# Kernel tuning notes

Measured on AMD Instinct MI355X. Metric: run time of the kernel, lower is better.

Reference implementation:

```python
import jax, jax.numpy as jnp
import numpy as np

DIM = 512
NUM_HEADS = 8
HEAD_DIM = DIM // NUM_HEADS
SCALE = HEAD_DIM ** -0.5
HIDDEN = int(DIM * 4.0)
LN_EPS = 1e-5


def layer_norm(x, w, b):
    mu = jnp.mean(x, axis=-1, keepdims=True)
    var = jnp.var(x, axis=-1, keepdims=True)
    return (x - mu) * jax.lax.rsqrt(var + LN_EPS) * w + b


def setup_inputs() -> dict:
    key = jax.random.key(0)
    ks = jax.random.split(key, 8)
    s = 0.02
    return {
        "x": jax.random.normal(ks[0], (8, 4096, DIM), dtype=jnp.float32),
        "ln1_w": jnp.ones((DIM,), jnp.float32),
        "ln1_b": jnp.zeros((DIM,), jnp.float32),
        "qkv_w": jax.random.normal(ks[1], (3 * DIM, DIM), jnp.float32) * s,
        "proj_w": jax.random.normal(ks[2], (DIM, DIM), jnp.float32) * s,
        "proj_b": jnp.zeros((DIM,), jnp.float32),
        "ln2_w": jnp.ones((DIM,), jnp.float32),
        "ln2_b": jnp.zeros((DIM,), jnp.float32),
        "fc1_w": jax.random.normal(ks[3], (HIDDEN, DIM), jnp.float32) * s,
        "fc1_b": jnp.zeros((HIDDEN,), jnp.float32),
        "fc2_w": jax.random.normal(ks[4], (DIM, HIDDEN), jnp.float32) * s,
        "fc2_b": jnp.zeros((DIM,), jnp.float32),
        "eca_w": jax.random.normal(ks[5], (1, 1, 3), jnp.float32) * 0.5,
    }


def channel_attention(x, qkv_w, proj_w, proj_b):
    B, N, C = x.shape
    qkv = (x @ qkv_w.T).reshape(B, N, 3, NUM_HEADS, HEAD_DIM)
    qkv = qkv.transpose(2, 0, 3, 1, 4)  # (3, B, h, N, hd)
    q, k, v = qkv[0], qkv[1] * SCALE, qkv[2]
    # cross-covariance attention: (hd x hd) per head
    attn = jax.nn.softmax(jnp.einsum("bhnd,bhne->bhde", k, v), axis=-1)
    out = jnp.einsum("bhde,bhne->bhnd", attn, q)  # (B, h, N, hd)
    out = out.transpose(0, 2, 1, 3).reshape(B, N, C)
    return out @ proj_w.T + proj_b


def mlp_eca(x, fc1_w, fc1_b, fc2_w, fc2_b, eca_w):
    B, N, C = x.shape
    H = W = int(np.sqrt(N))
    h = jax.nn.gelu(x @ fc1_w.T + fc1_b, approximate=False)
    y = h @ fc2_w.T + fc2_b  # (B, N, C)
    # faithful replication of torch .view(B, C, H, W) on contiguous (B, N, C)
    y4 = y.reshape(B, C, H, W)
    pooled = jnp.mean(y4, axis=(2, 3))  # (B, C)
    conv = jax.lax.conv_general_dilated(
        pooled[:, None, :], eca_w, window_strides=(1,), padding=[(1, 1)],
        dimension_numbers=("NCW", "OIW", "NCW"))[:, 0, :]  # (B, C)
    gate = jax.nn.sigmoid(conv)[:, :, None, None]
    y4 = y4 * gate + y4
    return y4.reshape(B, C, H * W).transpose(0, 2, 1)  # (B, N, C)


def reference(x, ln1_w, ln1_b, qkv_w, proj_w, proj_b, ln2_w, ln2_b,
              fc1_w, fc1_b, fc2_w, fc2_b, eca_w):
    cur = layer_norm(x, ln1_w, ln1_b)
    x = x + channel_attention(cur, qkv_w, proj_w, proj_b)
    x = x + mlp_eca(layer_norm(x, ln2_w, ln2_b), fc1_w, fc1_b, fc2_w, fc2_b, eca_w)
    return x
```

## Files before the change

### kernel.cpp

```cpp
#include <hip/hip_runtime.h>
#include <hip/hip_bf16.h>

typedef __bf16 bf16;
typedef __bf16 bf16x8 __attribute__((ext_vector_type(8)));
typedef float floatx4 __attribute__((ext_vector_type(4)));

#define B_    8
#define N_    4096
#define C_    512
#define BN_   32768
#define HID_  2048
#define SCALE_ 0.125f

__device__ __forceinline__ void load_lds16(const void* g, void* l) {
    __builtin_amdgcn_global_load_lds(
        (const __attribute__((address_space(1))) void*)g,
        (__attribute__((address_space(3))) void*)l, 16, 0, 0);
}

__global__ void sniff_kernel(const unsigned int* __restrict__ xw, int* __restrict__ flag)
{
    int t = threadIdx.x;
    int votes = 0;
#pragma unroll
    for (int i = 0; i < 4; i++) {
        unsigned w = xw[t * 4 + i];
        if (w == 0u) continue;
        unsigned a = w & 0xFFFFu;
        unsigned e = (a >> 7) & 0xFFu;
        if (a != 0u && e >= 110u && e <= 135u) votes++; else votes--;
    }
#pragma unroll
    for (int off = 32; off; off >>= 1) votes += __shfl_xor(votes, off);
    __shared__ int s[4];
    if ((t & 63) == 0) s[t >> 6] = votes;
    __syncthreads();
    if (t == 0) *flag = (s[0] + s[1] + s[2] + s[3]) > 0 ? 1 : 0;
}

struct ConvArgs {
    const void* src[12];
    unsigned    dstoff[12];
    int         n[12];
};

__global__ __launch_bounds__(256) void convert_params(
    ConvArgs args, char* __restrict__ ws, const int* __restrict__ flag)
{
    int seg = blockIdx.y;
    int n = args.n[seg];
    int base = blockIdx.x * 2048;
    if (base >= n) return;
    bf16* dst = (bf16*)(ws + args.dstoff[seg]);
    const void* src = args.src[seg];
    bool isbf = (*flag != 0);
#pragma unroll
    for (int j = 0; j < 8; j++) {
        int idx = base + threadIdx.x + j * 256;
        if (idx < n) {
            float v = isbf ? (float)((const bf16*)src)[idx]
                           : ((const float*)src)[idx];
            dst[idx] = (bf16)v;
        }
    }
}

__device__ __forceinline__ void ln_core(float f[8], const bf16* w, const bf16* b,
                                        int lane, bf16* outp)
{
    float s = 0.f, sq = 0.f;
#pragma unroll
    for (int j = 0; j < 8; j++) { s += f[j]; sq += f[j]*f[j]; }
#pragma unroll
    for (int off = 32; off; off >>= 1) { s += __shfl_xor(s, off); sq += __shfl_xor(sq, off); }
    float mean = s * (1.f/512.f);
    float var  = sq * (1.f/512.f) - mean*mean;
    float inv  = rsqrtf(var + 1e-5f);
    bf16x8 wv = *(const bf16x8*)(w + lane*8);
    bf16x8 bv = *(const bf16x8*)(b + lane*8);
    bf16x8 o;
#pragma unroll
    for (int j = 0; j < 8; j++) o[j] = (bf16)((f[j]-mean)*inv*(float)wv[j] + (float)bv[j]);
    *(bf16x8*)outp = o;
}

__global__ __launch_bounds__(256) void ln_dyn_kernel(
    const void* __restrict__ xv, const bf16* __restrict__ w,
    const bf16* __restrict__ b, bf16* __restrict__ out, const int* __restrict__ flag)
{
    int wave = threadIdx.x >> 6, lane = threadIdx.x & 63;
    size_t row = (size_t)blockIdx.x * 4 + wave;
    float f[8];
    if (*flag) {
        bf16x8 v = *(const bf16x8*)((const bf16*)xv + row * C_ + lane * 8);
#pragma unroll
        for (int j = 0; j < 8; j++) f[j] = (float)v[j];
    } else {
        const float4* p = (const float4*)((const float*)xv + row * C_ + lane * 8);
        float4 v0 = p[0], v1 = p[1];
        f[0]=v0.x; f[1]=v0.y; f[2]=v0.z; f[3]=v0.w;
        f[4]=v1.x; f[5]=v1.y; f[6]=v1.z; f[7]=v1.w;
    }
    ln_core(f, w, b, lane, out + row * C_ + lane*8);
}

__global__ __launch_bounds__(256) void ln_b16_kernel(
    const bf16* __restrict__ x, const bf16* __restrict__ w,
    const bf16* __restrict__ b, bf16* __restrict__ out)
{
    int wave = threadIdx.x >> 6, lane = threadIdx.x & 63;
    size_t row = (size_t)blockIdx.x * 4 + wave;
    bf16x8 v = *(const bf16x8*)(x + row * C_ + lane * 8);
    float f[8];
#pragma unroll
    for (int j = 0; j < 8; j++) f[j] = (float)v[j];
    ln_core(f, w, b, lane, out + row * C_ + lane*8);
}

__global__ __launch_bounds__(256) void ln_f32_kernel(
    const float* __restrict__ x, const bf16* __restrict__ w,
    const bf16* __restrict__ b, bf16* __restrict__ out)
{
    int wave = threadIdx.x >> 6, lane = threadIdx.x & 63;
    size_t row = (size_t)blockIdx.x * 4 + wave;
    const float4* p = (const float4*)(x + row * C_ + lane * 8);
    float4 v0 = p[0], v1 = p[1];
    float f[8] = { v0.x, v0.y, v0.z, v0.w, v1.x, v1.y, v1.z, v1.w };
    ln_core(f, w, b, lane, out + row * C_ + lane*8);
}

enum { EPI_NONE = 0, EPI_BIAS = 1, EPI_BIAS_RESID = 2, EPI_BIAS_GELU = 3, EPI_QKV = 4 };

__device__ __forceinline__ void stage_half(
    const bf16* __restrict__ G, int ldk, bf16* lbase, int t)
{
#pragma unroll
    for (int i = 0; i < 2; i++) {
        int c  = i * 512 + t;
        int r  = c >> 3;
        int ls = (c & 7) ^ (r & 7);
        load_lds16(G + (size_t)r * ldk + ls * 8, lbase + c * 8);
    }
}

#define LOAD_AF(half)                                                          \
    _Pragma("unroll") for (int mi = 0; mi < 4; mi++) {                         \
        int row = wm * 64 + mi * 16 + l16;                                     \
        _Pragma("unroll") for (int ks = 0; ks < 2; ks++)                       \
            af[mi][ks] = *(const bf16x8*)(&Asl[s][half][0][0] + row * 64 +     \
                ((ks * 32 + quad * 8) ^ ((row & 7) << 3)));                    \
    }
#define LOAD_BF(dst, half)                                                     \
    _Pragma("unroll") for (int ni = 0; ni < 2; ni++) {                         \
        int row = wn * 32 + ni * 16 + l16;                                     \
        _Pragma("unroll") for (int ks = 0; ks < 2; ks++)                       \
            dst[ni][ks] = *(const bf16x8*)(&Bsl[s][half][0][0] + row * 64 +    \
                ((ks * 32 + quad * 8) ^ ((row & 7) << 3)));                    \
    }
#define MFMA_Q(AH, BH, BFR)                                                    \
    __builtin_amdgcn_s_barrier();                                              \
    asm volatile("s_waitcnt lgkmcnt(0)");                                      \
    __builtin_amdgcn_s_setprio(1);                                             \
    _Pragma("unroll") for (int mi = 0; mi < 4; mi++)                           \
    _Pragma("unroll") for (int ni = 0; ni < 2; ni++)                           \
    _Pragma("unroll") for (int ks = 0; ks < 2; ks++)                           \
        acc[(AH)*4+mi][(BH)*2+ni] = __builtin_amdgcn_mfma_f32_16x16x32_bf16(   \
            af[mi][ks], BFR[ni][ks], acc[(AH)*4+mi][(BH)*2+ni], 0, 0, 0);      \
    __builtin_amdgcn_s_setprio(0);                                             \
    __builtin_amdgcn_s_barrier();

template<typename OutT, int EPI>
__global__ __launch_bounds__(512, 2) void gemm256(
    const bf16* __restrict__ A, const bf16* __restrict__ W,
    const bf16* __restrict__ bias, const void* __restrict__ resid,
    const int* __restrict__ flag,
    OutT* __restrict__ Cout, bf16* __restrict__ Cout2, int M, int Nn, int K)
{
    __shared__ bf16 Asl[2][2][128][64];
    __shared__ bf16 Bsl[2][2][128][64];
    const int t = threadIdx.x;
    const int wv = t >> 6, lane = t & 63;
    const int quad = lane >> 4, l16 = lane & 15;
    const int wm = wv >> 2, wn = wv & 3;
    const int Nt = Nn >> 8;
    const int id = blockIdx.x;
    const int xcd = id & 7, j = id >> 3;
    const int m0 = ((j / Nt) * 8 + xcd) * 256;
    const int n0 = (j % Nt) * 256;
    const int NKT = K >> 6;

    floatx4 acc[8][4] = {};
    bf16x8 af[4][2], bf0[2][2], bf1[2][2];

    stage_half(A + (size_t)m0 * K,           K, &Asl[0][0][0][0], t);
    stage_half(W + (size_t)n0 * K,           K, &Bsl[0][0][0][0], t);
    stage_half(A + (size_t)(m0 + 128) * K,   K, &Asl[0][1][0][0], t);
    stage_half(W + (size_t)(n0 + 128) * K,   K, &Bsl[0][1][0][0], t);
    stage_half(A + (size_t)m0 * K + 64,      K, &Asl[1][0][0][0], t);
    stage_half(W + (size_t)n0 * K + 64,      K, &Bsl[1][0][0][0], t);
    asm volatile("s_waitcnt vmcnt(4)");
    __builtin_amdgcn_s_barrier();

    for (int kt = 0; kt < NKT; ++kt) {
        const int s = kt & 1;
        LOAD_AF(0)
        LOAD_BF(bf0, 0)
        if (kt + 1 < NKT)
            stage_half(A + (size_t)(m0 + 128) * K + (size_t)(kt + 1) * 64, K,
                       &Asl[s ^ 1][1][0][0], t);
        MFMA_Q(0, 0, bf0)
        LOAD_BF(bf1, 1)
        if (kt + 1 < NKT)
            stage_half(W + (size_t)(n0 + 128) * K + (size_t)(kt + 1) * 64, K,
                       &Bsl[s ^ 1][1][0][0], t);
        MFMA_Q(0, 1, bf1)
        LOAD_AF(1)
        if (kt + 2 < NKT)
            stage_half(A + (size_t)m0 * K + (size_t)(kt + 2) * 64, K,
                       &Asl[s][0][0][0], t);
        MFMA_Q(1, 1, bf1)
        if (kt + 2 < NKT)
            stage_half(W + (size_t)n0 * K + (size_t)(kt + 2) * 64, K,
                       &Bsl[s][0][0][0], t);
        if (kt + 1 < NKT) {
            if (kt + 2 < NKT) asm volatile("s_waitcnt vmcnt(4)");
            else              asm volatile("s_waitcnt vmcnt(0)");
        }
        MFMA_Q(1, 0, bf0)
    }

    size_t ldc = (size_t)Nn; int csub = 0; bool to2 = false;
    if (EPI == EPI_QKV) {
        if (n0 >= 512) { to2 = true; ldc = 1024; csub = 512; }
        else           { ldc = 512; }
    }
    bool isbf = false;
    if (EPI == EPI_BIAS_RESID) isbf = (*flag != 0);

#pragma unroll
    for (int mg = 0; mg < 8; mg++) {
        int rowg = m0 + (mg >> 2) * 128 + wm * 64 + (mg & 3) * 16 + quad * 4;
#pragma unroll
        for (int ng = 0; ng < 4; ng++) {
            int col = n0 + (ng >> 1) * 128 + wn * 32 + (ng & 1) * 16 + l16;
            float bv = (EPI == EPI_BIAS || EPI == EPI_BIAS_RESID || EPI == EPI_BIAS_GELU)
                       ? (float)bias[col] : 0.f;
#pragma unroll
            for (int r = 0; r < 4; r++) {
                size_t idx = (size_t)(rowg + r) * ldc + (col - csub);
                float v = acc[mg][ng][r] + bv;
                if (EPI == EPI_BIAS_RESID) {
                    float rres = isbf ? (float)((const bf16*)resid)[idx]
                                      : ((const float*)resid)[idx];
                    v += rres;
                }
                if (EPI == EPI_BIAS_GELU)  v = 0.5f * v * (1.f + erff(v * 0.70710678118654752f));
                if (EPI == EPI_QKV && to2) Cout2[idx] = (bf16)v;
                else                       Cout[idx]  = (OutT)v;
            }
        }
    }
}

__global__ __launch_bounds__(256) void attn_logits_mfma(
    const bf16* __restrict__ kv, float* __restrict__ partial)
{
    __shared__ bf16 Kt[64][136];
    __shared__ bf16 Vt[64][136];
    int s = blockIdx.x, bh = blockIdx.y, b = bh >> 3, h = bh & 7;
    int t = threadIdx.x, wave = t >> 6, lane = t & 63;
    int quad = lane >> 4, l16 = lane & 15;
    floatx4 acc[4] = {};
    for (int c = 0; c < 4; c++) {
        int n0 = s * 512 + c * 128;
        {
            int isv = t >> 7;
            int r   = t & 127;
            const bf16* gp = &kv[((size_t)b * N_ + n0 + r) * 1024 + h * 64 + isv * 512];
            bf16x8 rowv[8];
#pragma unroll
            for (int u = 0; u < 8; u++) rowv[u] = *(const bf16x8*)(gp + u * 8);
            bf16 (*dst)[136] = isv ? Vt : Kt;
#pragma unroll
            for (int u = 0; u < 8; u++)
#pragma unroll
                for (int jj = 0; jj < 8; jj++)
                    dst[u * 8 + jj][r] = rowv[u][jj];
        }
        __syncthreads();
#pragma unroll
        for (int ks = 0; ks < 4; ks++) {
            bf16x8 af = *(const bf16x8*)&Kt[wave * 16 + l16][ks * 32 + quad * 8];
#pragma unroll
            for (int ni = 0; ni < 4; ni++) {
                bf16x8 bfv = *(const bf16x8*)&Vt[ni * 16 + l16][ks * 32 + quad * 8];
                acc[ni] = __builtin_amdgcn_mfma_f32_16x16x32_bf16(af, bfv, acc[ni], 0, 0, 0);
            }
        }
        __syncthreads();
    }
    float* p = partial + ((size_t)bh * 8 + s) * 4096;
#pragma unroll
    for (int ni = 0; ni < 4; ni++)
#pragma unroll
        for (int r = 0; r < 4; r++)
            p[(wave * 16 + quad * 4 + r) * 64 + ni * 16 + l16] = acc[ni][r];
}

__global__ __launch_bounds__(256) void attn_softmax_kernel(
    const float* __restrict__ partial, bf16* __restrict__ attnb)
{
    int bh = blockIdx.y;
    int wave = threadIdx.x >> 6, lane = threadIdx.x & 63;
    for (int r = 0; r < 4; r++) {
        int d = blockIdx.x * 16 + wave * 4 + r;
        float v = 0.f;
#pragma unroll
        for (int s = 0; s < 8; s++) v += partial[((size_t)bh*8 + s)*4096 + d*64 + lane];
        v *= SCALE_;
        float m = v;
#pragma unroll
        for (int off = 32; off; off >>= 1) m = fmaxf(m, __shfl_xor(m, off));
        float p = expf(v - m);
        float sum = p;
#pragma unroll
        for (int off = 32; off; off >>= 1) sum += __shfl_xor(sum, off);
        attnb[(size_t)bh*4096 + d*64 + lane] = (bf16)(p / sum);
    }
}

__global__ __launch_bounds__(256) void attn_apply_mfma(
    const bf16* __restrict__ q, const bf16* __restrict__ attnb,
    bf16* __restrict__ outT)
{
    int bh = blockIdx.y, b = bh >> 3, h = bh & 7;
    int t = threadIdx.x, wave = t >> 6, lane = t & 63;
    int quad = lane >> 4, l16 = lane & 15;
    int nbase = blockIdx.x * 256 + wave * 64;
    bf16x8 bfrag[4][2];
#pragma unroll
    for (int di = 0; di < 4; di++)
#pragma unroll
        for (int ks = 0; ks < 2; ks++)
            bfrag[di][ks] = *(const bf16x8*)&attnb[(size_t)bh*4096 + (di*16 + l16)*64 + ks*32 + quad*8];
    floatx4 acc[4][4] = {};
#pragma unroll
    for (int mi = 0; mi < 4; mi++) {
#pragma unroll
        for (int ks = 0; ks < 2; ks++) {
            bf16x8 af = *(const bf16x8*)&q[((size_t)b*N_ + nbase + mi*16 + l16)*512 + h*64 + ks*32 + quad*8];
#pragma unroll
            for (int di = 0; di < 4; di++)
                acc[mi][di] = __builtin_amdgcn_mfma_f32_16x16x32_bf16(af, bfrag[di][ks], acc[mi][di], 0, 0, 0);
        }
    }
#pragma unroll
    for (int mi = 0; mi < 4; mi++)
#pragma unroll
        for (int di = 0; di < 4; di++)
#pragma unroll
            for (int r = 0; r < 4; r++)
                outT[((size_t)b*N_ + nbase + mi*16 + quad*4 + r)*512 + h*64 + di*16 + l16] =
                    (bf16)acc[mi][di][r];
}

__global__ __launch_bounds__(256) void pooled_kernel(
    const bf16* __restrict__ y, float* __restrict__ pooled)
{
    int bc = blockIdx.x;
    const bf16* p = y + (size_t)bc * 4096 + threadIdx.x * 16;
    float s = 0.f;
#pragma unroll
    for (int i = 0; i < 2; i++) {
        bf16x8 v = *(const bf16x8*)(p + i*8);
#pragma unroll
        for (int j = 0; j < 8; j++) s += (float)v[j];
    }
#pragma unroll
    for (int off = 32; off; off >>= 1) s += __shfl_xor(s, off);
    __shared__ float red[4];
    if ((threadIdx.x & 63) == 0) red[threadIdx.x >> 6] = s;
    __syncthreads();
    if (threadIdx.x == 0)
        pooled[bc] = (red[0] + red[1] + red[2] + red[3]) * (1.f/4096.f);
}

__global__ void gate_kernel(const float* __restrict__ pooled,
                            const bf16* __restrict__ eca_w, float* __restrict__ gate1)
{
    int c = threadIdx.x, b = blockIdx.x;
    float w0 = (float)eca_w[0], w1 = (float)eca_w[1], w2 = (float)eca_w[2];
    const float* p = pooled + b * 512;
    float conv = w1 * p[c];
    if (c > 0)   conv += w0 * p[c-1];
    if (c < 511) conv += w2 * p[c+1];
    float g = 1.f / (1.f + expf(-conv));
    gate1[b * 512 + c] = 1.f + g;
}

__global__ __launch_bounds__(256) void final_rmw(
    const bf16* __restrict__ y, const float* __restrict__ gate1,
    float* __restrict__ out)
{
    int b = blockIdx.z, c0 = blockIdx.y * 64, n0 = blockIdx.x * 64;
    __shared__ float ytile[64][65];
    int t = threadIdx.x;
#pragma unroll
    for (int i = 0; i < 2; i++) {
        int chunk = t * 2 + i;
        int ci = chunk >> 3, nj = (chunk & 7) * 8;
        bf16x8 v = *(const bf16x8*)&y[(size_t)b * ((size_t)N_*C_) + (size_t)(c0+ci) * 4096 + n0 + nj];
#pragma unroll
        for (int j = 0; j < 8; j++) ytile[ci][nj+j] = (float)v[j];
    }
    __syncthreads();
    int cc = t & 63, nb = t >> 6;
    float g = gate1[b * 512 + c0 + cc];
    for (int p = 0; p < 16; p++) {
        int nr = p * 4 + nb;
        size_t idx = ((size_t)b * N_ + n0 + nr) * C_ + c0 + cc;
        out[idx] = out[idx] + g * ytile[cc][nr];
    }
}

__global__ __launch_bounds__(256) void final_fresh(
    const bf16* __restrict__ y, const bf16* __restrict__ x2b,
    const float* __restrict__ gate1, float* __restrict__ out)
{
    int b = blockIdx.z, c0 = blockIdx.y * 64, n0 = blockIdx.x * 64;
    __shared__ float ytile[64][65];
    int t = threadIdx.x;
#pragma unroll
    for (int i = 0; i < 2; i++) {
        int chunk = t * 2 + i;
        int ci = chunk >> 3, nj = (chunk & 7) * 8;
        bf16x8 v = *(const bf16x8*)&y[(size_t)b * ((size_t)N_*C_) + (size_t)(c0+ci) * 4096 + n0 + nj];
#pragma unroll
        for (int j = 0; j < 8; j++) ytile[ci][nj+j] = (float)v[j];
    }
    __syncthreads();
    int cc = t & 63, nb = t >> 6;
    float g = gate1[b * 512 + c0 + cc];
    for (int p = 0; p < 16; p++) {
        int nr = p * 4 + nb;
        size_t idx = ((size_t)b * N_ + n0 + nr) * C_ + c0 + cc;
        out[idx] = (float)x2b[idx] + g * ytile[cc][nr];
    }
}

extern "C" void kernel_launch(void* const* d_in, const int* in_sizes, int n_in,
                              void* d_out, int out_size, void* d_ws, size_t ws_size,
                              hipStream_t stream)
{
    float* outf = (float*)d_out;
    bf16*  outb = (bf16*)d_out;
    char* ws = (char*)d_ws;

    int*   flag    = (int*)ws;
    float* pooled  = (float*)(ws + 4096);
    float* gate1   = (float*)(ws + 20480);
    bf16* ln1_w = (bf16*)(ws + 65536);
    bf16* ln1_b = (bf16*)(ws + 67584);
    bf16* ln2_w = (bf16*)(ws + 69632);
    bf16* ln2_b = (bf16*)(ws + 71680);
    bf16* proj_b= (bf16*)(ws + 73728);
    bf16* fc2_b = (bf16*)(ws + 75776);
    bf16* eca_w = (bf16*)(ws + 77824);
    bf16* fc1_b = (bf16*)(ws + 81920);
    bf16* qkv_w = (bf16*)(ws + ((size_t)1 << 20));
    bf16* proj_w= (bf16*)(ws + (size_t)2621440);
    bf16* fc1_w = (bf16*)(ws + ((size_t)3 << 20));
    bf16* fc2_w = (bf16*)(ws + ((size_t)5 << 20));
    float* partial = (float*)(ws + ((size_t)7  << 20));
    bf16*  attnb   = (bf16*)(ws + ((size_t)15 << 20));
    bf16*  T1      = (bf16*)(ws + ((size_t)16 << 20));
    bf16*  kvbuf   = (bf16*)(ws + ((size_t)48 << 20));
    bf16*  hbuf    = kvbuf;
    bf16*  x2b     = (bf16*)(ws + ((size_t)176 << 20));

    const bool fat = ws_size >= ((size_t)212 << 20);

    sniff_kernel<<<1, 256, 0, stream>>>((const unsigned int*)d_in[0], flag);

    ConvArgs ca;
    const int   srcidx[12] = { 1, 2, 6, 7, 5, 11, 12, 9, 3, 4, 8, 10 };
    const unsigned offs[12] = { 65536, 67584, 69632, 71680, 73728, 75776, 77824, 81920,
                                1u<<20, 2621440u, 3u<<20, 5u<<20 };
    for (int i = 0; i < 12; i++) {
        ca.src[i] = d_in[srcidx[i]];
        ca.dstoff[i] = offs[i];
        ca.n[i] = in_sizes[srcidx[i]];
    }
    convert_params<<<dim3(512, 12), 256, 0, stream>>>(ca, ws, flag);

    ln_dyn_kernel<<<BN_/4, 256, 0, stream>>>(d_in[0], ln1_w, ln1_b, T1, flag);

    gemm256<bf16, EPI_QKV><<<768, 512, 0, stream>>>(
        T1, qkv_w, nullptr, nullptr, flag, outb, kvbuf, BN_, 1536, 512);

    attn_logits_mfma<<<dim3(8, 64), 256, 0, stream>>>(kvbuf, partial);
    attn_softmax_kernel<<<dim3(4, 64), 256, 0, stream>>>(partial, attnb);
    attn_apply_mfma<<<dim3(16, 64), 256, 0, stream>>>(outb, attnb, T1);

    if (fat) {
        gemm256<bf16, EPI_BIAS_RESID><<<256, 512, 0, stream>>>(
            T1, proj_w, proj_b, d_in[0], flag, x2b, nullptr, BN_, 512, 512);
        ln_b16_kernel<<<BN_/4, 256, 0, stream>>>(x2b, ln2_w, ln2_b, T1);
        gemm256<bf16, EPI_BIAS_GELU><<<1024, 512, 0, stream>>>(
            T1, fc1_w, fc1_b, nullptr, flag, hbuf, nullptr, BN_, 2048, 512);
        gemm256<bf16, EPI_BIAS><<<256, 512, 0, stream>>>(
            hbuf, fc2_w, fc2_b, nullptr, flag, T1, nullptr, BN_, 512, 2048);
        pooled_kernel<<<4096, 256, 0, stream>>>(T1, pooled);
        gate_kernel<<<8, 512, 0, stream>>>(pooled, eca_w, gate1);
        final_fresh<<<dim3(64, 8, 8), 256, 0, stream>>>(T1, x2b, gate1, outf);
    } else {
        gemm256<float, EPI_BIAS_RESID><<<256, 512, 0, stream>>>(
            T1, proj_w, proj_b, d_in[0], flag, outf, nullptr, BN_, 512, 512);
        ln_f32_kernel<<<BN_/4, 256, 0, stream>>>(outf, ln2_w, ln2_b, T1);
        for (int ch = 0; ch < 2; ch++) {
            bf16* Tch = T1 + (size_t)ch * 16384 * 512;
            gemm256<bf16, EPI_BIAS_GELU><<<512, 512, 0, stream>>>(
                Tch, fc1_w, fc1_b, nullptr, flag, hbuf, nullptr, 16384, 2048, 512);
            gemm256<bf16, EPI_BIAS><<<128, 512, 0, stream>>>(
                hbuf, fc2_w, fc2_b, nullptr, flag, Tch, nullptr, 16384, 512, 2048);
        }
        pooled_kernel<<<4096, 256, 0, stream>>>(T1, pooled);
        gate_kernel<<<8, 512, 0, stream>>>(pooled, eca_w, gate1);
        final_rmw<<<dim3(64, 8, 8), 256, 0, stream>>>(T1, gate1, outf);
    }
}
```

Measured before the change: 549.9 us.

## Make GEMM persistent with cross-tile prefetch and use tanh-form GELU

```diff
diff --git a/kernel.cpp b/kernel.cpp
--- a/kernel.cpp
+++ b/kernel.cpp
@@ -16,6 +16,12 @@
     __builtin_amdgcn_global_load_lds(
         (const __attribute__((address_space(1))) void*)g,
         (__attribute__((address_space(3))) void*)l, 16, 0, 0);
+}
+
+__device__ __forceinline__ float gelu_fast(float v) {
+    float c = fmaf(v * v, 0.044715f, 1.0f) * v;
+    float e = __builtin_amdgcn_exp2f(-2.3022082f * c);
+    return v * __builtin_amdgcn_rcpf(1.0f + e);
 }
 
 __global__ void sniff_kernel(const unsigned int* __restrict__ xw, int* __restrict__ flag)
@@ -183,14 +189,14 @@
     const int quad = lane >> 4, l16 = lane & 15;
     const int wm = wv >> 2, wn = wv & 3;
     const int Nt = Nn >> 8;
-    const int id = blockIdx.x;
-    const int xcd = id & 7, j = id >> 3;
-    const int m0 = ((j / Nt) * 8 + xcd) * 256;
-    const int n0 = (j % Nt) * 256;
+    const int total = (M >> 8) * Nt;
+    const int G = gridDim.x;
     const int NKT = K >> 6;
 
-    floatx4 acc[8][4] = {};
-    bf16x8 af[4][2], bf0[2][2], bf1[2][2];
+    int id = blockIdx.x;
+    if (id >= total) return;
+    int m0 = (((id >> 3) / Nt) * 8 + (id & 7)) * 256;
+    int n0 = ((id >> 3) % Nt) * 256;
 
     stage_half(A + (size_t)m0 * K,           K, &Asl[0][0][0][0], t);
     stage_half(W + (size_t)n0 * K,           K, &Bsl[0][0][0][0], t);
@@ -201,64 +207,92 @@
     asm volatile("s_waitcnt vmcnt(4)");
     __builtin_amdgcn_s_barrier();
 
-    for (int kt = 0; kt < NKT; ++kt) {
-        const int s = kt & 1;
-        LOAD_AF(0)
-        LOAD_BF(bf0, 0)
-        if (kt + 1 < NKT)
-            stage_half(A + (size_t)(m0 + 128) * K + (size_t)(kt + 1) * 64, K,
-                       &Asl[s ^ 1][1][0][0], t);
-        MFMA_Q(0, 0, bf0)
-        LOAD_BF(bf1, 1)
-        if (kt + 1 < NKT)
-            stage_half(W + (size_t)(n0 + 128) * K + (size_t)(kt + 1) * 64, K,
-                       &Bsl[s ^ 1][1][0][0], t);
-        MFMA_Q(0, 1, bf1)
-        LOAD_AF(1)
-        if (kt + 2 < NKT)
-            stage_half(A + (size_t)m0 * K + (size_t)(kt + 2) * 64, K,
-                       &Asl[s][0][0][0], t);
-        MFMA_Q(1, 1, bf1)
-        if (kt + 2 < NKT)
-            stage_half(W + (size_t)n0 * K + (size_t)(kt + 2) * 64, K,
-                       &Bsl[s][0][0][0], t);
-        if (kt + 1 < NKT) {
-            if (kt + 2 < NKT) asm volatile("s_waitcnt vmcnt(4)");
-            else              asm volatile("s_waitcnt vmcnt(0)");
-        }
-        MFMA_Q(1, 0, bf0)
-    }
-
-    size_t ldc = (size_t)Nn; int csub = 0; bool to2 = false;
-    if (EPI == EPI_QKV) {
-        if (n0 >= 512) { to2 = true; ldc = 1024; csub = 512; }
-        else           { ldc = 512; }
-    }
-    bool isbf = false;
-    if (EPI == EPI_BIAS_RESID) isbf = (*flag != 0);
-
-#pragma unroll
-    for (int mg = 0; mg < 8; mg++) {
-        int rowg = m0 + (mg >> 2) * 128 + wm * 64 + (mg & 3) * 16 + quad * 4;
-#pragma unroll
-        for (int ng = 0; ng < 4; ng++) {
-            int col = n0 + (ng >> 1) * 128 + wn * 32 + (ng & 1) * 16 + l16;
-            float bv = (EPI == EPI_BIAS || EPI == EPI_BIAS_RESID || EPI == EPI_BIAS_GELU)
-                       ? (float)bias[col] : 0.f;
-#pragma unroll
-            for (int r = 0; r < 4; r++) {
-                size_t idx = (size_t)(rowg + r) * ldc + (col - csub);
-                float v = acc[mg][ng][r] + bv;
-                if (EPI == EPI_BIAS_RESID) {
-                    float rres = isbf ? (float)((const bf16*)resid)[idx]
-                                      : ((const float*)resid)[idx];
-                    v += rres;
+    for (;;) {
+        const int idn = id + G;
+        const bool hn = idn < total;
+        int m0n = 0, n0n = 0;
+        if (hn) {
+            m0n = (((idn >> 3) / Nt) * 8 + (idn & 7)) * 256;
+            n0n = ((idn >> 3) % Nt) * 256;
+        }
+
+        floatx4 acc[8][4] = {};
+        bf16x8 af[4][2], bf0[2][2], bf1[2][2];
+
+        for (int kt = 0; kt < NKT; ++kt) {
+            const int s = kt & 1;
+            LOAD_AF(0)
+            LOAD_BF(bf0, 0)
+            {
+                const bf16* p = (kt + 1 < NKT)
+                    ? A + (size_t)(m0 + 128) * K + (size_t)(kt + 1) * 64
+                    : (hn ? A + (size_t)(m0n + 128) * K : nullptr);
+                if (p) stage_half(p, K, &Asl[s ^ 1][1][0][0], t);
+            }
+            MFMA_Q(0, 0, bf0)
+            LOAD_BF(bf1, 1)
+            {
+                const bf16* p = (kt + 1 < NKT)
+                    ? W + (size_t)(n0 + 128) * K + (size_t)(kt + 1) * 64
+                    : (hn ? W + (size_t)(n0n + 128) * K : nullptr);
+                if (p) stage_half(p, K, &Bsl[s ^ 1][1][0][0], t);
+            }
+            MFMA_Q(0, 1, bf1)
+            LOAD_AF(1)
+            {
+                const bf16* p = (kt + 2 < NKT)
+                    ? A + (size_t)m0 * K + (size_t)(kt + 2) * 64
+                    : (hn ? A + (size_t)m0n * K + (size_t)(kt + 2 - NKT) * 64 : nullptr);
+                if (p) stage_half(p, K, &Asl[s][0][0][0], t);
+            }
+            MFMA_Q(1, 1, bf1)
+            {
+                const bf16* p = (kt + 2 < NKT)
+                    ? W + (size_t)n0 * K + (size_t)(kt + 2) * 64
+                    : (hn ? W + (size_t)n0n * K + (size_t)(kt + 2 - NKT) * 64 : nullptr);
+                if (p) stage_half(p, K, &Bsl[s][0][0][0], t);
+            }
+            if (kt + 1 < NKT || hn) {
+                if (kt + 2 < NKT || hn) asm volatile("s_waitcnt vmcnt(4)");
+                else                    asm volatile("s_waitcnt vmcnt(0)");
+            }
+            MFMA_Q(1, 0, bf0)
+        }
+
+        size_t ldc = (size_t)Nn; int csub = 0; bool to2 = false;
+        if (EPI == EPI_QKV) {
+            if (n0 >= 512) { to2 = true; ldc = 1024; csub = 512; }
+            else           { ldc = 512; }
+        }
+        bool isbf = false;
+        if (EPI == EPI_BIAS_RESID) isbf = (*flag != 0);
+
+#pragma unroll
+        for (int mg = 0; mg < 8; mg++) {
+            int rowg = m0 + (mg >> 2) * 128 + wm * 64 + (mg & 3) * 16 + quad * 4;
+#pragma unroll
+            for (int ng = 0; ng < 4; ng++) {
+                int col = n0 + (ng >> 1) * 128 + wn * 32 + (ng & 1) * 16 + l16;
+                float bv = (EPI == EPI_BIAS || EPI == EPI_BIAS_RESID || EPI == EPI_BIAS_GELU)
+                           ? (float)bias[col] : 0.f;
+#pragma unroll
+                for (int r = 0; r < 4; r++) {
+                    size_t idx = (size_t)(rowg + r) * ldc + (col - csub);
+                    float v = acc[mg][ng][r] + bv;
+                    if (EPI == EPI_BIAS_RESID) {
+                        float rres = isbf ? (float)((const bf16*)resid)[idx]
+                                          : ((const float*)resid)[idx];
+                        v += rres;
+                    }
+                    if (EPI == EPI_BIAS_GELU)  v = gelu_fast(v);
+                    if (EPI == EPI_QKV && to2) Cout2[idx] = (bf16)v;
+                    else                       Cout[idx]  = (OutT)v;
                 }
-                if (EPI == EPI_BIAS_GELU)  v = 0.5f * v * (1.f + erff(v * 0.70710678118654752f));
-                if (EPI == EPI_QKV && to2) Cout2[idx] = (bf16)v;
-                else                       Cout[idx]  = (OutT)v;
-            }
-        }
+            }
+        }
+
+        if (!hn) break;
+        id = idn; m0 = m0n; n0 = n0n;
     }
 }
 
@@ -495,7 +529,7 @@
 
     ln_dyn_kernel<<<BN_/4, 256, 0, stream>>>(d_in[0], ln1_w, ln1_b, T1, flag);
 
-    gemm256<bf16, EPI_QKV><<<768, 512, 0, stream>>>(
+    gemm256<bf16, EPI_QKV><<<256, 512, 0, stream>>>(
         T1, qkv_w, nullptr, nullptr, flag, outb, kvbuf, BN_, 1536, 512);
 
     attn_logits_mfma<<<dim3(8, 64), 256, 0, stream>>>(kvbuf, partial);
@@ -506,7 +540,7 @@
         gemm256<bf16, EPI_BIAS_RESID><<<256, 512, 0, stream>>>(
             T1, proj_w, proj_b, d_in[0], flag, x2b, nullptr, BN_, 512, 512);
         ln_b16_kernel<<<BN_/4, 256, 0, stream>>>(x2b, ln2_w, ln2_b, T1);
-        gemm256<bf16, EPI_BIAS_GELU><<<1024, 512, 0, stream>>>(
+        gemm256<bf16, EPI_BIAS_GELU><<<256, 512, 0, stream>>>(
             T1, fc1_w, fc1_b, nullptr, flag, hbuf, nullptr, BN_, 2048, 512);
         gemm256<bf16, EPI_BIAS><<<256, 512, 0, stream>>>(
             hbuf, fc2_w, fc2_b, nullptr, flag, T1, nullptr, BN_, 512, 2048);
@@ -519,7 +553,7 @@
         ln_f32_kernel<<<BN_/4, 256, 0, stream>>>(outf, ln2_w, ln2_b, T1);
         for (int ch = 0; ch < 2; ch++) {
             bf16* Tch = T1 + (size_t)ch * 16384 * 512;
-            gemm256<bf16, EPI_BIAS_GELU><<<512, 512, 0, stream>>>(
+            gemm256<bf16, EPI_BIAS_GELU><<<256, 512, 0, stream>>>(
                 Tch, fc1_w, fc1_b, nullptr, flag, hbuf, nullptr, 16384, 2048, 512);
             gemm256<bf16, EPI_BIAS><<<128, 512, 0, stream>>>(
                 hbuf, fc2_w, fc2_b, nullptr, flag, Tch, nullptr, 16384, 512, 2048);
```

Result: faster. 529.9 us (-3.6%).
